# Kernel tuning notes

Measured on AMD Instinct MI355X. Metric: run time of the kernel, lower is better.

Reference implementation:

```python
import jax, jax.numpy as jnp
import numpy as np

B, C, E, H = 8, 2048, 1024, 128


def setup_inputs() -> dict:
    key = jax.random.key(0)
    k1, k2, k3, k4 = jax.random.split(key, 4)
    x = jax.random.normal(k1, (B, C, E), dtype=jnp.float32)
    # store projection weights as (E, H) so projection is x @ W
    Wq = jax.random.normal(k2, (E, H), dtype=jnp.float32) * (E ** -0.5)
    Wk = jax.random.normal(k3, (E, H), dtype=jnp.float32) * (E ** -0.5)
    Wv = jax.random.normal(k4, (E, H), dtype=jnp.float32) * (E ** -0.5)
    return {"x": x, "Wq": Wq, "Wk": Wk, "Wv": Wv}


def reference(x, Wq, Wk, Wv):
    # x: (B, C, E) -> out: (B, C, H)
    _, c, e = x.shape
    q = x @ Wq  # (B, C, H)
    k = x @ Wk  # (B, C, H)
    v = x @ Wv  # (B, C, H)
    # NOTE: original scales by embed_size**0.5, not head_size**0.5
    scale = jnp.asarray(e, x.dtype) ** 0.5
    w = jnp.einsum('bqh,bkh->bqk', q, k) / scale  # (B, C, C)
    causal = jnp.tril(jnp.ones((c, c), dtype=bool))
    w = jnp.where(causal, w, -jnp.inf)
    w = jax.nn.softmax(w, axis=-1)
    # dropout_rate = 0.0 -> identity (eval mode)
    out = w @ v  # (B, C, H)
    return out
```

## Files before the change

### kernel.cpp

```cpp
#include <hip/hip_runtime.h>
#include <hip/hip_bf16.h>
#include <stdint.h>

#define B_ 8
#define C_ 2048
#define E_ 1024
#define H_ 128
#define M_ (B_*C_)
#define SLOTS_B 144

typedef __attribute__((ext_vector_type(8))) short bf16x8;
typedef __attribute__((ext_vector_type(4))) float f32x4;

__device__ __forceinline__ unsigned short f2bf(float f) {
    union { float f; unsigned int u; } v; v.f = f;
    unsigned int u = v.u;
    u += 0x7fff + ((u >> 16) & 1);
    return (unsigned short)(u >> 16);
}
__device__ __forceinline__ float bf2f(unsigned short u) {
    union { unsigned int i; float f; } v; v.i = ((unsigned int)u) << 16; return v.f;
}
__device__ __forceinline__ unsigned int pack2bf(float lo, float hi) {
    union { float f; unsigned int u; } a, b; a.f = lo; b.f = hi;
    return __builtin_amdgcn_perm(b.u + 0x8000u, a.u + 0x8000u, 0x07060302);
}

#define GLOAD_LDS16(g, l) \
    __builtin_amdgcn_global_load_lds((const __attribute__((address_space(1))) void*)(g), \
                                     (__attribute__((address_space(3))) void*)(l), 16, 0, 0)

__global__ __launch_bounds__(256) void wt2_kernel(const float* __restrict__ Wq,
                                                  const float* __restrict__ Wk,
                                                  const float* __restrict__ Wv,
                                                  unsigned short* __restrict__ WT2) {
    int z = blockIdx.y;
    const float* W = (z == 0) ? Wq : (z == 1) ? Wk : Wv;
    unsigned short* o = WT2 + (size_t)z * H_ * E_;
    int gid = blockIdx.x * 256 + threadIdx.x;
    int g = gid >> 7, h = gid & 127;
    unsigned short t[8];
#pragma unroll
    for (int j = 0; j < 8; ++j)
        t[j] = f2bf(W[(size_t)(g * 8 + j) * H_ + h]);
    *(bf16x8*)&o[(size_t)(g * 128 + h) * 8] = *(const bf16x8*)t;
}

#define MF(a, b, c) __builtin_amdgcn_mfma_f32_16x16x32_bf16((a), (b), (c), 0, 0, 0)

__global__ __launch_bounds__(256) void proj_kernel(const float* __restrict__ x,
                                                   const unsigned short* __restrict__ WT2,
                                                   unsigned short* __restrict__ QKV) {
    __shared__ __align__(16) float Asf[2][32][64];

    const int tid = threadIdx.x;
    const int wid = tid >> 6, lane = tid & 63;
    const int lrow = lane & 15, lq = lane >> 4;
    const int wcol = wid * 32;
    const int row0 = blockIdx.x * 32;
    const int w = blockIdx.y;
    const unsigned short* wbase = WT2 + (size_t)w * H_ * E_
                                + (size_t)(lq * 128 + wcol + lrow) * 8;

    const int srow = tid >> 4;
    const int sp = tid & 15;
    const int sg = sp >> 1, sh = sp & 1;

    auto ASTAGE = [&](int buf, int t) {
#pragma unroll
        for (int s = 0; s < 2; ++s) {
            int row = s * 16 + srow;
            const float* src = x + (size_t)(row0 + row) * E_ + t * 64
                             + ((sg ^ (row & 7)) * 8 + sh * 4);
            GLOAD_LDS16(src, (char*)&Asf[buf][0][0] + s * 4096 + tid * 16);
        }
    };

    f32x4 acc[2][2];
#pragma unroll
    for (int mi = 0; mi < 2; ++mi)
#pragma unroll
        for (int ni = 0; ni < 2; ++ni) acc[mi][ni] = (f32x4){0.f, 0.f, 0.f, 0.f};

    ASTAGE(0, 0);

    for (int t = 0; t < 16; ++t) {
        const int cur = t & 1;
        __syncthreads();
        if (t < 15) ASTAGE(cur ^ 1, t + 1);

        bf16x8 bfr[2][2];
#pragma unroll
        for (int ks = 0; ks < 2; ++ks)
#pragma unroll
            for (int ni = 0; ni < 2; ++ni)
                bfr[ks][ni] = *(const bf16x8*)(wbase + (size_t)t * 8192 + ks * 4096 + ni * 128);

        bf16x8 af[2][2];
#pragma unroll
        for (int mi = 0; mi < 2; ++mi)
#pragma unroll
            for (int ks = 0; ks < 2; ++ks) {
                int row = mi * 16 + lrow;
                int gL = (ks * 4 + lq) ^ (row & 7);
                const float* ap = &Asf[cur][row][gL * 8];
                f32x4 f0 = *(const f32x4*)ap;
                f32x4 f1 = *(const f32x4*)(ap + 4);
                union { unsigned int u[4]; bf16x8 v; } pk;
                pk.u[0] = pack2bf(f0[0], f0[1]);
                pk.u[1] = pack2bf(f0[2], f0[3]);
                pk.u[2] = pack2bf(f1[0], f1[1]);
                pk.u[3] = pack2bf(f1[2], f1[3]);
                af[mi][ks] = pk.v;
            }
#pragma unroll
        for (int ks = 0; ks < 2; ++ks)
#pragma unroll
            for (int mi = 0; mi < 2; ++mi)
#pragma unroll
                for (int ni = 0; ni < 2; ++ni)
                    acc[mi][ni] = MF(af[mi][ks], bfr[ks][ni], acc[mi][ni]);
    }

    if (w < 2) {
        const float qs = (w == 0) ? 0.03125f : 1.0f;
        unsigned short* outp = QKV + (size_t)w * M_ * H_;
#pragma unroll
        for (int mi = 0; mi < 2; ++mi) {
            int r0 = row0 + mi * 16 + lq * 4;
#pragma unroll
            for (int ni = 0; ni < 2; ++ni) {
                int col = wcol + ni * 16 + lrow;
#pragma unroll
                for (int r = 0; r < 4; ++r)
                    outp[(size_t)(r0 + r) * H_ + col] = f2bf(acc[mi][ni][r] * qs);
            }
        }
    } else {
        unsigned short* vt = QKV + (size_t)2 * M_ * H_;
        int b = row0 / C_;
        int cbase = row0 % C_;
#pragma unroll
        for (int mi = 0; mi < 2; ++mi) {
            int c0 = cbase + mi * 16 + lq * 4;
#pragma unroll
            for (int ni = 0; ni < 2; ++ni) {
                int h = wcol + ni * 16 + lrow;
                __align__(8) unsigned short p[4] = {f2bf(acc[mi][ni][0]), f2bf(acc[mi][ni][1]),
                                                    f2bf(acc[mi][ni][2]), f2bf(acc[mi][ni][3])};
                *(uint2*)&vt[((size_t)b * H_ + h) * C_ + c0] = *(const uint2*)p;
            }
        }
    }
}

__global__ __launch_bounds__(256) void attn_kernel(const unsigned short* __restrict__ QKV,
                                                   unsigned short* __restrict__ PO,
                                                   float* __restrict__ ML,
                                                   float* __restrict__ out) {
    __shared__ __align__(16) unsigned short Ks[2][64][128];
    __shared__ __align__(16) unsigned short Vt[2][128][64];

    const unsigned short* Q  = QKV;
    const unsigned short* K  = QKV + (size_t)M_ * H_;
    const unsigned short* VT = QKV + (size_t)2 * M_ * H_;

    const int tid = threadIdx.x, wid = tid >> 6, lane = tid & 63;
    const int lrow = lane & 15, lq = lane >> 4, lk = lq * 8;
    const int b = blockIdx.x;
    const int rr = blockIdx.y;

    int j = 0;
#pragma unroll
    for (int jj = 1; jj < 32; ++jj) {
        int q = jj >> 2, s = jj & 3;
        if (jj + 2 * q * (q - 1) + s * q <= rr) j = jj;
    }
    const int qj = j >> 2, sj = j & 3;
    const int Cj = j + 2 * qj * (qj - 1) + sj * qj;
    const int c = rr - Cj;
    const int nch = qj + 1;
    const int t0 = c * 4;
    const int t1 = min(t0 + 4, j + 1);

    const int q0w = j * 64 + wid * 16;
    const unsigned short* Kb  = K  + (size_t)b * C_ * H_;
    const unsigned short* VTb = VT + (size_t)b * H_ * C_;
    const int qabs = q0w + lrow;

    const int krow = tid >> 4, kg = tid & 15;
    const int vrow = tid >> 3, vg = tid & 7;

    bf16x8 qf[4];
#pragma unroll
    for (int kf = 0; kf < 4; ++kf)
        qf[kf] = *(const bf16x8*)&Q[((size_t)b * C_ + q0w + lrow) * H_ + kf * 32 + lk];

    f32x4 o[8];
#pragma unroll
    for (int nf = 0; nf < 8; ++nf) o[nf] = (f32x4){0.f, 0.f, 0.f, 0.f};
    float m = -INFINITY, l = 0.f;

    auto STAGE = [&](int buf, int t) {
        const int kv0 = t * 64;
#pragma unroll
        for (int s = 0; s < 4; ++s) {
            int r = s * 16 + krow;
            int prow = ((r & 0x10) << 1) | ((r & 0x0C) << 1) | ((r & 0x20) >> 3) | (r & 3);
            GLOAD_LDS16(&Kb[(size_t)(kv0 + prow) * H_ + ((kg ^ (r & 15)) * 8)],
                        (char*)&Ks[buf][0][0] + s * 4096 + tid * 16);
        }
#pragma unroll
        for (int s = 0; s < 4; ++s) {
            int h = s * 32 + vrow;
            GLOAD_LDS16(&VTb[(size_t)h * C_ + kv0 + ((vg ^ (h & 7)) * 8)],
                        (char*)&Vt[buf][0][0] + s * 4096 + tid * 16);
        }
    };

    STAGE(0, t0);

    for (int t = t0; t < t1; ++t) {
        const int cur = (t - t0) & 1;
        __syncthreads();
        if (t + 1 < t1) STAGE(cur ^ 1, t + 1);

        const int kv0 = t * 64;
        f32x4 s[4];
        __builtin_amdgcn_s_setprio(1);
#pragma unroll
        for (int nf = 0; nf < 4; ++nf) {
            s[nf] = (f32x4){0.f, 0.f, 0.f, 0.f};
            const int rk = nf * 16 + lrow;
#pragma unroll
            for (int kf = 0; kf < 4; ++kf) {
                bf16x8 kb = *(const bf16x8*)&Ks[cur][rk][((kf * 4 + lq) ^ (rk & 15)) * 8];
                s[nf] = __builtin_amdgcn_mfma_f32_16x16x32_bf16(kb, qf[kf], s[nf], 0, 0, 0);
            }
        }
        __builtin_amdgcn_s_setprio(0);
        bf16x8 vb[8][2];
#pragma unroll
        for (int nf = 0; nf < 8; ++nf) {
            const int h = nf * 16 + lrow;
#pragma unroll
            for (int kf2 = 0; kf2 < 2; ++kf2)
                vb[nf][kf2] = *(const bf16x8*)&Vt[cur][h][((kf2 * 4 + lq) ^ (h & 7)) * 8];
        }

        if (t == j) {
#pragma unroll
            for (int nf = 0; nf < 4; ++nf) {
                int kvb = kv0 + ((nf & 1) << 5) + (lq << 3) + ((nf >> 1) << 2);
#pragma unroll
                for (int r = 0; r < 4; ++r)
                    if (kvb + r > qabs) s[nf][r] = -INFINITY;
            }
        }
        float mt = s[0][0];
#pragma unroll
        for (int nf = 0; nf < 4; ++nf)
#pragma unroll
            for (int r = 0; r < 4; ++r) mt = fmaxf(mt, s[nf][r]);
        mt = fmaxf(mt, __shfl_xor(mt, 16));
        mt = fmaxf(mt, __shfl_xor(mt, 32));

        float mn = fmaxf(m, mt);
        float corr = __expf(m - mn);
        m = mn;

        float p[4][4];
        float ps = 0.f;
#pragma unroll
        for (int nf = 0; nf < 4; ++nf)
#pragma unroll
            for (int r = 0; r < 4; ++r) {
                float e = __expf(s[nf][r] - mn);
                p[nf][r] = e;
                ps += e;
            }
        ps += __shfl_xor(ps, 16);
        ps += __shfl_xor(ps, 32);
        l = l * corr + ps;

        float corr4[4];
#pragma unroll
        for (int r = 0; r < 4; ++r)
            corr4[r] = __shfl(corr, (lane & 48) | (lq * 4 + r));
#pragma unroll
        for (int nf = 0; nf < 8; ++nf)
#pragma unroll
            for (int r = 0; r < 4; ++r) o[nf][r] *= corr4[r];

        bf16x8 pa[2];
#pragma unroll
        for (int kf2 = 0; kf2 < 2; ++kf2) {
            union { unsigned int u[4]; bf16x8 v; } pk;
            pk.u[0] = pack2bf(p[kf2][0],     p[kf2][1]);
            pk.u[1] = pack2bf(p[kf2][2],     p[kf2][3]);
            pk.u[2] = pack2bf(p[kf2 + 2][0], p[kf2 + 2][1]);
            pk.u[3] = pack2bf(p[kf2 + 2][2], p[kf2 + 2][3]);
            pa[kf2] = pk.v;
        }
        __builtin_amdgcn_s_setprio(1);
#pragma unroll
        for (int nf = 0; nf < 8; ++nf)
#pragma unroll
            for (int kf2 = 0; kf2 < 2; ++kf2)
                o[nf] = __builtin_amdgcn_mfma_f32_16x16x32_bf16(pa[kf2], vb[nf][kf2], o[nf], 0, 0, 0);
        __builtin_amdgcn_s_setprio(0);
    }

    float l4[4], m4[4];
#pragma unroll
    for (int r = 0; r < 4; ++r) {
        l4[r] = __shfl(l, (lane & 48) | (lq * 4 + r));
        m4[r] = __shfl(m, (lane & 48) | (lq * 4 + r));
    }
    const int qrow0 = q0w + lq * 4;

    if (nch == 1) {
#pragma unroll
        for (int nf = 0; nf < 8; ++nf) {
            int col = nf * 16 + lrow;
#pragma unroll
            for (int r = 0; r < 4; ++r)
                out[((size_t)b * C_ + qrow0 + r) * H_ + col] = o[nf][r] / l4[r];
        }
    } else {
        const int slot = b * SLOTS_B + rr;
        unsigned short* po = PO + (size_t)slot * 64 * 128;
        const int rl0 = wid * 16 + lq * 4;
#pragma unroll
        for (int nf = 0; nf < 8; ++nf) {
            int col = nf * 16 + lrow;
#pragma unroll
            for (int r = 0; r < 4; ++r)
                po[(size_t)(rl0 + r) * 128 + col] = f2bf(o[nf][r]);
        }
        if (lrow == 0) {
            float* ml = ML + (size_t)slot * 128;
#pragma unroll
            for (int r = 0; r < 4; ++r) {
                ml[rl0 + r] = m4[r];
                ml[64 + rl0 + r] = l4[r];
            }
        }
    }
}

__global__ __launch_bounds__(256) void combine_kernel(const unsigned short* __restrict__ PO,
                                                      const float* __restrict__ ML,
                                                      float* __restrict__ out) {
    const int j = blockIdx.x + 4;
    const int b = blockIdx.y;
    const int q = j >> 2, s = j & 3;
    const int Cj = j + 2 * q * (q - 1) + s * q;
    const int nch = q + 1;
    const int base = b * SLOTS_B + Cj;
    const int row = threadIdx.x >> 2;
    const int colg = (threadIdx.x & 3) * 32;

    float mstar = -INFINITY;
    for (int c = 0; c < nch; ++c)
        mstar = fmaxf(mstar, ML[(size_t)(base + c) * 128 + row]);

    float denom = 0.f;
    float acc[32];
#pragma unroll
    for (int i = 0; i < 32; ++i) acc[i] = 0.f;

    for (int c = 0; c < nch; ++c) {
        float mc = ML[(size_t)(base + c) * 128 + row];
        float lc = ML[(size_t)(base + c) * 128 + 64 + row];
        float w = __expf(mc - mstar);
        denom += w * lc;
        const unsigned short* p = PO + (size_t)(base + c) * 64 * 128 + (size_t)row * 128 + colg;
#pragma unroll
        for (int k = 0; k < 4; ++k) {
            bf16x8 v = *(const bf16x8*)&p[k * 8];
#pragma unroll
            for (int e = 0; e < 8; ++e)
                acc[k * 8 + e] += w * bf2f(((unsigned short*)&v)[e]);
        }
    }
    float inv = 1.f / denom;
    float* op = out + ((size_t)b * C_ + j * 64 + row) * H_ + colg;
#pragma unroll
    for (int k = 0; k < 8; ++k) {
        float4 st = {acc[k * 4] * inv, acc[k * 4 + 1] * inv, acc[k * 4 + 2] * inv, acc[k * 4 + 3] * inv};
        *(float4*)&op[k * 4] = st;
    }
}

extern "C" void kernel_launch(void* const* d_in, const int* in_sizes, int n_in,
                              void* d_out, int out_size, void* d_ws, size_t ws_size,
                              hipStream_t stream) {
    const float* x  = (const float*)d_in[0];
    const float* Wq = (const float*)d_in[1];
    const float* Wk = (const float*)d_in[2];
    const float* Wv = (const float*)d_in[3];
    float* out = (float*)d_out;

    unsigned short* WT2 = (unsigned short*)d_ws;
    unsigned short* QKV = WT2 + (size_t)3 * H_ * E_;
    unsigned short* PO  = QKV + (size_t)3 * M_ * H_;
    float*          ML  = (float*)(PO + (size_t)8 * SLOTS_B * 64 * 128);

    wt2_kernel<<<dim3(E_ / 8 * H_ / 256, 3), 256, 0, stream>>>(Wq, Wk, Wv, WT2);
    proj_kernel<<<dim3(M_ / 32, 3), 256, 0, stream>>>(x, WT2, QKV);
    attn_kernel<<<dim3(B_, SLOTS_B), 256, 0, stream>>>(QKV, PO, ML, out);
    combine_kernel<<<dim3(28, B_), 256, 0, stream>>>(PO, ML, out);
}
```

Measured before the change: 77.88 us.

## Stage projection weights in LDS with larger 64-row tiles and triple-buffered x

The projection kernel now processes 64 rows per block instead of 32, with a 2x2 wave layout in which each wave computes a 32x64 output tile. Weight tiles are staged into swizzled LDS through async global-to-LDS loads rather than read directly from global memory by each wave. The x tile now uses three buffers with a prefetch distance of two and a manual vmcnt wait before the barrier. The weight-transpose kernel is simplified to a plain row-major transpose. The aim is to raise weight reuse and hide load latency, at the cost of much more LDS per block and lower occupancy.

```diff
diff --git a/kernel.cpp b/kernel.cpp
--- a/kernel.cpp
+++ b/kernel.cpp
@@ -30,96 +30,103 @@
     __builtin_amdgcn_global_load_lds((const __attribute__((address_space(1))) void*)(g), \
                                      (__attribute__((address_space(3))) void*)(l), 16, 0, 0)
 
-__global__ __launch_bounds__(256) void wt2_kernel(const float* __restrict__ Wq,
-                                                  const float* __restrict__ Wk,
-                                                  const float* __restrict__ Wv,
-                                                  unsigned short* __restrict__ WT2) {
+__global__ __launch_bounds__(256) void wt_kernel(const float* __restrict__ Wq,
+                                                 const float* __restrict__ Wk,
+                                                 const float* __restrict__ Wv,
+                                                 unsigned short* __restrict__ WT) {
     int z = blockIdx.y;
     const float* W = (z == 0) ? Wq : (z == 1) ? Wk : Wv;
-    unsigned short* o = WT2 + (size_t)z * H_ * E_;
-    int gid = blockIdx.x * 256 + threadIdx.x;
-    int g = gid >> 7, h = gid & 127;
-    unsigned short t[8];
-#pragma unroll
-    for (int j = 0; j < 8; ++j)
-        t[j] = f2bf(W[(size_t)(g * 8 + j) * H_ + h]);
-    *(bf16x8*)&o[(size_t)(g * 128 + h) * 8] = *(const bf16x8*)t;
+    unsigned short* o = WT + (size_t)z * H_ * E_;
+    int idx = blockIdx.x * 256 + threadIdx.x;
+    int e = idx & (E_ - 1), h = idx >> 10;
+    o[(size_t)h * E_ + e] = f2bf(W[(size_t)e * H_ + h]);
 }
 
 #define MF(a, b, c) __builtin_amdgcn_mfma_f32_16x16x32_bf16((a), (b), (c), 0, 0, 0)
 
 __global__ __launch_bounds__(256) void proj_kernel(const float* __restrict__ x,
-                                                   const unsigned short* __restrict__ WT2,
+                                                   const unsigned short* __restrict__ WT,
                                                    unsigned short* __restrict__ QKV) {
-    __shared__ __align__(16) float Asf[2][32][64];
+    __shared__ __align__(16) float Asf[3][64][64];
+    __shared__ __align__(16) unsigned short Bs[2][128][64];
 
     const int tid = threadIdx.x;
     const int wid = tid >> 6, lane = tid & 63;
     const int lrow = lane & 15, lq = lane >> 4;
-    const int wcol = wid * 32;
-    const int row0 = blockIdx.x * 32;
+    const int wr = wid >> 1, wc = wid & 1;
+    const int row0 = blockIdx.x * 64;
     const int w = blockIdx.y;
-    const unsigned short* wbase = WT2 + (size_t)w * H_ * E_
-                                + (size_t)(lq * 128 + wcol + lrow) * 8;
+    const unsigned short* wt = WT + (size_t)w * H_ * E_;
 
     const int srow = tid >> 4;
-    const int sp = tid & 15;
-    const int sg = sp >> 1, sh = sp & 1;
+    const int slotL = tid & 15;
 
     auto ASTAGE = [&](int buf, int t) {
 #pragma unroll
-        for (int s = 0; s < 2; ++s) {
+        for (int s = 0; s < 4; ++s) {
             int row = s * 16 + srow;
             const float* src = x + (size_t)(row0 + row) * E_ + t * 64
-                             + ((sg ^ (row & 7)) * 8 + sh * 4);
+                             + ((slotL ^ (row & 7)) * 4);
             GLOAD_LDS16(src, (char*)&Asf[buf][0][0] + s * 4096 + tid * 16);
         }
     };
-
-    f32x4 acc[2][2];
+    auto BSTAGE = [&](int buf, int t) {
+#pragma unroll
+        for (int s = 0; s < 4; ++s) {
+            int brow = s * 32 + (tid >> 3);
+            int bg = (tid & 7) ^ (brow & 7);
+            GLOAD_LDS16(wt + (size_t)brow * E_ + t * 64 + bg * 8,
+                        (char*)&Bs[buf][0][0] + s * 4096 + tid * 16);
+        }
+    };
+
+    f32x4 acc[2][4];
 #pragma unroll
     for (int mi = 0; mi < 2; ++mi)
 #pragma unroll
-        for (int ni = 0; ni < 2; ++ni) acc[mi][ni] = (f32x4){0.f, 0.f, 0.f, 0.f};
-
+        for (int ni = 0; ni < 4; ++ni) acc[mi][ni] = (f32x4){0.f, 0.f, 0.f, 0.f};
+
+    BSTAGE(0, 0);
     ASTAGE(0, 0);
-
+    ASTAGE(1, 1);
+
+    int a0 = 0, a1 = 1, a2 = 2;
     for (int t = 0; t < 16; ++t) {
-        const int cur = t & 1;
-        __syncthreads();
-        if (t < 15) ASTAGE(cur ^ 1, t + 1);
-
-        bf16x8 bfr[2][2];
-#pragma unroll
-        for (int ks = 0; ks < 2; ++ks)
-#pragma unroll
-            for (int ni = 0; ni < 2; ++ni)
-                bfr[ks][ni] = *(const bf16x8*)(wbase + (size_t)t * 8192 + ks * 4096 + ni * 128);
-
-        bf16x8 af[2][2];
-#pragma unroll
-        for (int mi = 0; mi < 2; ++mi)
-#pragma unroll
-            for (int ks = 0; ks < 2; ++ks) {
-                int row = mi * 16 + lrow;
-                int gL = (ks * 4 + lq) ^ (row & 7);
-                const float* ap = &Asf[cur][row][gL * 8];
-                f32x4 f0 = *(const f32x4*)ap;
-                f32x4 f1 = *(const f32x4*)(ap + 4);
+        const int bb = t & 1;
+        asm volatile("s_waitcnt vmcnt(4)\n\ts_barrier" ::: "memory");
+        __builtin_amdgcn_sched_barrier(0);
+        BSTAGE(bb ^ 1, min(t + 1, 15));
+        ASTAGE(a2, min(t + 2, 15));
+
+#pragma unroll
+        for (int ks = 0; ks < 2; ++ks) {
+            const int g2 = (ks * 4 + lq) * 2;
+            bf16x8 af[2], bfr[4];
+#pragma unroll
+            for (int mi = 0; mi < 2; ++mi) {
+                int row = wr * 32 + mi * 16 + lrow;
+                int m7 = row & 7;
+                f32x4 f0 = *(const f32x4*)&Asf[a0][row][(g2 ^ m7) * 4];
+                f32x4 f1 = *(const f32x4*)&Asf[a0][row][((g2 + 1) ^ m7) * 4];
                 union { unsigned int u[4]; bf16x8 v; } pk;
                 pk.u[0] = pack2bf(f0[0], f0[1]);
                 pk.u[1] = pack2bf(f0[2], f0[3]);
                 pk.u[2] = pack2bf(f1[0], f1[1]);
                 pk.u[3] = pack2bf(f1[2], f1[3]);
-                af[mi][ks] = pk.v;
-            }
-#pragma unroll
-        for (int ks = 0; ks < 2; ++ks)
+                af[mi] = pk.v;
+            }
+#pragma unroll
+            for (int ni = 0; ni < 4; ++ni) {
+                int rb = wc * 64 + ni * 16 + lrow;
+                bfr[ni] = *(const bf16x8*)&Bs[bb][rb][((ks * 4 + lq) ^ (rb & 7)) * 8];
+            }
 #pragma unroll
             for (int mi = 0; mi < 2; ++mi)
 #pragma unroll
-                for (int ni = 0; ni < 2; ++ni)
-                    acc[mi][ni] = MF(af[mi][ks], bfr[ks][ni], acc[mi][ni]);
+                for (int ni = 0; ni < 4; ++ni)
+                    acc[mi][ni] = MF(af[mi], bfr[ni], acc[mi][ni]);
+        }
+        int tmp = a0; a0 = a1; a1 = a2; a2 = tmp;
     }
 
     if (w < 2) {
@@ -127,10 +134,10 @@
         unsigned short* outp = QKV + (size_t)w * M_ * H_;
 #pragma unroll
         for (int mi = 0; mi < 2; ++mi) {
-            int r0 = row0 + mi * 16 + lq * 4;
-#pragma unroll
-            for (int ni = 0; ni < 2; ++ni) {
-                int col = wcol + ni * 16 + lrow;
+            int r0 = row0 + wr * 32 + mi * 16 + lq * 4;
+#pragma unroll
+            for (int ni = 0; ni < 4; ++ni) {
+                int col = wc * 64 + ni * 16 + lrow;
 #pragma unroll
                 for (int r = 0; r < 4; ++r)
                     outp[(size_t)(r0 + r) * H_ + col] = f2bf(acc[mi][ni][r] * qs);
@@ -142,10 +149,10 @@
         int cbase = row0 % C_;
 #pragma unroll
         for (int mi = 0; mi < 2; ++mi) {
-            int c0 = cbase + mi * 16 + lq * 4;
-#pragma unroll
-            for (int ni = 0; ni < 2; ++ni) {
-                int h = wcol + ni * 16 + lrow;
+            int c0 = cbase + wr * 32 + mi * 16 + lq * 4;
+#pragma unroll
+            for (int ni = 0; ni < 4; ++ni) {
+                int h = wc * 64 + ni * 16 + lrow;
                 __align__(8) unsigned short p[4] = {f2bf(acc[mi][ni][0]), f2bf(acc[mi][ni][1]),
                                                     f2bf(acc[mi][ni][2]), f2bf(acc[mi][ni][3])};
                 *(uint2*)&vt[((size_t)b * H_ + h) * C_ + c0] = *(const uint2*)p;
@@ -402,13 +409,13 @@
     const float* Wv = (const float*)d_in[3];
     float* out = (float*)d_out;
 
-    unsigned short* WT2 = (unsigned short*)d_ws;
-    unsigned short* QKV = WT2 + (size_t)3 * H_ * E_;
+    unsigned short* WT  = (unsigned short*)d_ws;
+    unsigned short* QKV = WT + (size_t)3 * H_ * E_;
     unsigned short* PO  = QKV + (size_t)3 * M_ * H_;
     float*          ML  = (float*)(PO + (size_t)8 * SLOTS_B * 64 * 128);
 
-    wt2_kernel<<<dim3(E_ / 8 * H_ / 256, 3), 256, 0, stream>>>(Wq, Wk, Wv, WT2);
-    proj_kernel<<<dim3(M_ / 32, 3), 256, 0, stream>>>(x, WT2, QKV);
+    wt_kernel<<<dim3(H_ * E_ / 256, 3), 256, 0, stream>>>(Wq, Wk, Wv, WT);
+    proj_kernel<<<dim3(M_ / 64, 3), 256, 0, stream>>>(x, WT, QKV);
     attn_kernel<<<dim3(B_, SLOTS_B), 256, 0, stream>>>(QKV, PO, ML, out);
     combine_kernel<<<dim3(28, B_), 256, 0, stream>>>(PO, ML, out);
 }
```

New measurement: 92.00 us. +18.1%, slower.

## Fuse Q/K/V projections into one block and triple-buffer x staging

Applied to the files above, without the earlier changes.

The projection kernel now computes all three Q, K and V outputs in a single block per 32-row tile instead of launching one block per weight matrix, so each x tile is read from global memory and converted to bf16 once rather than three times. The x staging moves from double to triple buffering with an explicit vmcnt wait plus barrier, which keeps two loads in flight. MFMA sections also get raised wave priority. The cost is more accumulator and weight-fragment registers per thread and a third as many blocks, which may lower occupancy and reduce latency hiding.

```diff
diff --git a/kernel.cpp b/kernel.cpp
--- a/kernel.cpp
+++ b/kernel.cpp
@@ -51,50 +51,54 @@
 __global__ __launch_bounds__(256) void proj_kernel(const float* __restrict__ x,
                                                    const unsigned short* __restrict__ WT2,
                                                    unsigned short* __restrict__ QKV) {
-    __shared__ __align__(16) float Asf[2][32][64];
+    __shared__ __align__(16) float Asf[3][32][64];
 
     const int tid = threadIdx.x;
     const int wid = tid >> 6, lane = tid & 63;
     const int lrow = lane & 15, lq = lane >> 4;
     const int wcol = wid * 32;
     const int row0 = blockIdx.x * 32;
-    const int w = blockIdx.y;
-    const unsigned short* wbase = WT2 + (size_t)w * H_ * E_
-                                + (size_t)(lq * 128 + wcol + lrow) * 8;
+    const unsigned short* wbase = WT2 + (size_t)(lq * 128 + wcol + lrow) * 8;
 
     const int srow = tid >> 4;
-    const int sp = tid & 15;
-    const int sg = sp >> 1, sh = sp & 1;
+    const int slotL = tid & 15;
 
     auto ASTAGE = [&](int buf, int t) {
 #pragma unroll
         for (int s = 0; s < 2; ++s) {
             int row = s * 16 + srow;
             const float* src = x + (size_t)(row0 + row) * E_ + t * 64
-                             + ((sg ^ (row & 7)) * 8 + sh * 4);
+                             + ((slotL ^ (row & 7)) * 4);
             GLOAD_LDS16(src, (char*)&Asf[buf][0][0] + s * 4096 + tid * 16);
         }
     };
 
-    f32x4 acc[2][2];
-#pragma unroll
-    for (int mi = 0; mi < 2; ++mi)
-#pragma unroll
-        for (int ni = 0; ni < 2; ++ni) acc[mi][ni] = (f32x4){0.f, 0.f, 0.f, 0.f};
+    f32x4 acc[3][2][2];
+#pragma unroll
+    for (int w = 0; w < 3; ++w)
+#pragma unroll
+        for (int mi = 0; mi < 2; ++mi)
+#pragma unroll
+            for (int ni = 0; ni < 2; ++ni) acc[w][mi][ni] = (f32x4){0.f, 0.f, 0.f, 0.f};
 
     ASTAGE(0, 0);
+    ASTAGE(1, 1);
 
     for (int t = 0; t < 16; ++t) {
-        const int cur = t & 1;
-        __syncthreads();
-        if (t < 15) ASTAGE(cur ^ 1, t + 1);
-
-        bf16x8 bfr[2][2];
-#pragma unroll
-        for (int ks = 0; ks < 2; ++ks)
-#pragma unroll
-            for (int ni = 0; ni < 2; ++ni)
-                bfr[ks][ni] = *(const bf16x8*)(wbase + (size_t)t * 8192 + ks * 4096 + ni * 128);
+        const int a0 = t % 3;
+        asm volatile("s_waitcnt vmcnt(2)\n\ts_barrier" ::: "memory");
+        __builtin_amdgcn_sched_barrier(0);
+        if (t < 15) ASTAGE((t + 2) % 3, min(t + 2, 15));
+
+        bf16x8 bw[3][2][2];
+        const unsigned short* wp = wbase + (size_t)t * 8192;
+#pragma unroll
+        for (int w = 0; w < 3; ++w)
+#pragma unroll
+            for (int ks = 0; ks < 2; ++ks)
+#pragma unroll
+                for (int ni = 0; ni < 2; ++ni)
+                    bw[w][ks][ni] = *(const bf16x8*)(wp + (size_t)w * 131072 + ks * 4096 + ni * 128);
 
         bf16x8 af[2][2];
 #pragma unroll
@@ -102,10 +106,10 @@
 #pragma unroll
             for (int ks = 0; ks < 2; ++ks) {
                 int row = mi * 16 + lrow;
-                int gL = (ks * 4 + lq) ^ (row & 7);
-                const float* ap = &Asf[cur][row][gL * 8];
-                f32x4 f0 = *(const f32x4*)ap;
-                f32x4 f1 = *(const f32x4*)(ap + 4);
+                int m7 = row & 7;
+                int s0 = 2 * (ks * 4 + lq);
+                f32x4 f0 = *(const f32x4*)&Asf[a0][row][((s0)     ^ m7) * 4];
+                f32x4 f1 = *(const f32x4*)&Asf[a0][row][((s0 + 1) ^ m7) * 4];
                 union { unsigned int u[4]; bf16x8 v; } pk;
                 pk.u[0] = pack2bf(f0[0], f0[1]);
                 pk.u[1] = pack2bf(f0[2], f0[3]);
@@ -113,16 +117,22 @@
                 pk.u[3] = pack2bf(f1[2], f1[3]);
                 af[mi][ks] = pk.v;
             }
+
+        __builtin_amdgcn_s_setprio(1);
 #pragma unroll
         for (int ks = 0; ks < 2; ++ks)
 #pragma unroll
-            for (int mi = 0; mi < 2; ++mi)
+            for (int w = 0; w < 3; ++w)
 #pragma unroll
                 for (int ni = 0; ni < 2; ++ni)
-                    acc[mi][ni] = MF(af[mi][ks], bfr[ks][ni], acc[mi][ni]);
-    }
-
-    if (w < 2) {
+#pragma unroll
+                    for (int mi = 0; mi < 2; ++mi)
+                        acc[w][mi][ni] = MF(af[mi][ks], bw[w][ks][ni], acc[w][mi][ni]);
+        __builtin_amdgcn_s_setprio(0);
+    }
+
+#pragma unroll
+    for (int w = 0; w < 2; ++w) {
         const float qs = (w == 0) ? 0.03125f : 1.0f;
         unsigned short* outp = QKV + (size_t)w * M_ * H_;
 #pragma unroll
@@ -133,10 +143,11 @@
                 int col = wcol + ni * 16 + lrow;
 #pragma unroll
                 for (int r = 0; r < 4; ++r)
-                    outp[(size_t)(r0 + r) * H_ + col] = f2bf(acc[mi][ni][r] * qs);
-            }
-        }
-    } else {
+                    outp[(size_t)(r0 + r) * H_ + col] = f2bf(acc[w][mi][ni][r] * qs);
+            }
+        }
+    }
+    {
         unsigned short* vt = QKV + (size_t)2 * M_ * H_;
         int b = row0 / C_;
         int cbase = row0 % C_;
@@ -146,8 +157,8 @@
 #pragma unroll
             for (int ni = 0; ni < 2; ++ni) {
                 int h = wcol + ni * 16 + lrow;
-                __align__(8) unsigned short p[4] = {f2bf(acc[mi][ni][0]), f2bf(acc[mi][ni][1]),
-                                                    f2bf(acc[mi][ni][2]), f2bf(acc[mi][ni][3])};
+                __align__(8) unsigned short p[4] = {f2bf(acc[2][mi][ni][0]), f2bf(acc[2][mi][ni][1]),
+                                                    f2bf(acc[2][mi][ni][2]), f2bf(acc[2][mi][ni][3])};
                 *(uint2*)&vt[((size_t)b * H_ + h) * C_ + c0] = *(const uint2*)p;
             }
         }
@@ -408,7 +419,7 @@
     float*          ML  = (float*)(PO + (size_t)8 * SLOTS_B * 64 * 128);
 
     wt2_kernel<<<dim3(E_ / 8 * H_ / 256, 3), 256, 0, stream>>>(Wq, Wk, Wv, WT2);
-    proj_kernel<<<dim3(M_ / 32, 3), 256, 0, stream>>>(x, WT2, QKV);
+    proj_kernel<<<dim3(M_ / 32), 256, 0, stream>>>(x, WT2, QKV);
     attn_kernel<<<dim3(B_, SLOTS_B), 256, 0, stream>>>(QKV, PO, ML, out);
     combine_kernel<<<dim3(28, B_), 256, 0, stream>>>(PO, ML, out);
 }
```

Result: faster. 71.98 us (-7.6%).
